# Kernel optimization log

Hardware: AMD Instinct MI355X
Metric: run time of the kernel (lower is better)

The kernel has to match this reference:

```python
import jax, jax.numpy as jnp
import numpy as np

LN_EPS = 1e-5
NEG_INF = -1e30


def setup_inputs() -> dict:
    key = jax.random.key(0)
    k_adj, k_feat, k_mask, k_w = jax.random.split(key, 4)
    B, N, H, R, L = 8, 400, 768, 46, 2
    adj = jax.random.uniform(k_adj, (B, N, N, R), dtype=jnp.float32)
    feature = jax.random.normal(k_feat, (B, N, H), dtype=jnp.float32)
    dmask = (jax.random.uniform(k_mask, (B, 1, N)) > 0.1).astype(jnp.float32)
    # per-layer, per-relation Linear(H, H, bias=False) weights, applied as x @ W
    W = jax.random.normal(k_w, (L, R, H, H), dtype=jnp.float32) / np.sqrt(H)
    return {"adj": adj, "feature": feature, "dmask": dmask, "W": W}


def reference(adj, feature, dmask, W):
    # adj: [B,N,N,R] -> [B,R,N,N]; dmask: [B,1,N] masks key/column axis
    B, N, _, R = adj.shape
    a = jnp.transpose(adj, (0, 3, 1, 2))           # [B,R,N,N]
    m = dmask[:, None, :, :]                        # [B,1,1,N]
    logits = a * m + (1.0 - m) * NEG_INF
    att = jax.nn.softmax(logits, axis=-1)           # [B,R,N,N] (layer-invariant)

    x = feature
    num_layers = W.shape[0]
    for layer in range(num_layers):
        # grouped per-relation linear: h[b,r,n,k] = feature[b,n,h] @ W[layer,r,h,k]
        h = jnp.einsum('bnh,rhk->brnk', x, W[layer])
        h = jax.nn.relu(jnp.einsum('brnm,brmk->brnk', att, h))
        addition = h.sum(axis=1)                    # sum over relations -> [B,N,H]
        z = jax.nn.relu(addition) / R
        # LayerNorm without affine params
        mu = jnp.mean(z, axis=-1, keepdims=True)
        var = jnp.var(z, axis=-1, keepdims=True)
        x = (z - mu) / jnp.sqrt(var + LN_EPS)
        # dropout is identity in eval mode
    return x
```

## Files before the change

### kernel.cpp

```cpp
#include <hip/hip_runtime.h>
#include <stdint.h>

#define BS 8
#define NN 400
#define HH 768
#define RR 46
#define MB 416
#define APAD 448
#define MFLAT2 3328
#define LDW2 3328
#define PADM 402

typedef _Float16 half8 __attribute__((ext_vector_type(8)));
typedef _Float16 half4v __attribute__((ext_vector_type(4)));
typedef float floatx4 __attribute__((ext_vector_type(4)));

__device__ __forceinline__ void async16(const void* g, void* l) {
  __builtin_amdgcn_global_load_lds((const __attribute__((address_space(1))) uint32_t*)g,
                                   (__attribute__((address_space(3))) uint32_t*)l, 16, 0, 0);
}

__device__ __forceinline__ int xcd_work(int flat, int nwg) {
  int q = nwg >> 3, rem = nwg & 7;
  int xcd = flat & 7, slot = flat >> 3;
  return (xcd < rem ? xcd * (q + 1) : rem * (q + 1) + (xcd - rem) * q) + slot;
}

__device__ __forceinline__ void vm_wait(int ahead) {
  if (ahead >= 2) asm volatile("s_waitcnt vmcnt(8)" ::: "memory");
  else if (ahead == 1) asm volatile("s_waitcnt vmcnt(4)" ::: "memory");
  else asm volatile("s_waitcnt vmcnt(0)" ::: "memory");
}
__device__ __forceinline__ void vm_wait3(int ahead) {
  if (ahead >= 2) asm volatile("s_waitcnt vmcnt(6)" ::: "memory");
  else if (ahead == 1) asm volatile("s_waitcnt vmcnt(3)" ::: "memory");
  else asm volatile("s_waitcnt vmcnt(0)" ::: "memory");
}
#define BAR_ONE() { asm volatile("s_barrier" ::: "memory"); __builtin_amdgcn_sched_barrier(0); }


__device__ __forceinline__ void mma_tiles(const _Float16* As, const _Float16* Bs, int lane,
                                          int wr, int wc, floatx4 acc[4][4]) {
  int arow = wr + (lane & 15);
  int brow = wc + (lane & 15);
  int kswz = ((lane >> 4) ^ ((lane >> 1) & 3)) * 8;
  half8 a[4], b[4];
#pragma unroll
  for (int i = 0; i < 4; ++i) a[i] = *(const half8*)&As[(arow + i * 16) * 32 + kswz];
#pragma unroll
  for (int i = 0; i < 4; ++i) b[i] = *(const half8*)&Bs[(brow + i * 16) * 32 + kswz];
#pragma unroll
  for (int i = 0; i < 4; ++i)
#pragma unroll
    for (int j = 0; j < 4; ++j)
      acc[i][j] = __builtin_amdgcn_mfma_f32_16x16x32_f16(a[i], b[j], acc[i][j], 0, 0, 0);
}

__device__ __forceinline__ void mma32(const _Float16* As, const _Float16* Bs, int lane,
                                      int wr, int wc, floatx4 acc[8][4]) {
  int arow = wr + (lane & 15);
  int brow = wc + (lane & 15);
  int kswz = ((lane >> 4) ^ ((lane >> 1) & 3)) * 8;
  half8 a[8], b[4];
#pragma unroll
  for (int i = 0; i < 8; ++i) a[i] = *(const half8*)&As[(arow + i * 16) * 32 + kswz];
#pragma unroll
  for (int j = 0; j < 4; ++j) b[j] = *(const half8*)&Bs[(brow + j * 16) * 32 + kswz];
#pragma unroll
  for (int i = 0; i < 8; ++i)
#pragma unroll
    for (int j = 0; j < 4; ++j)
      acc[i][j] = __builtin_amdgcn_mfma_f32_16x16x32_f16(a[i], b[j], acc[i][j], 0, 0, 0);
}

__global__ __launch_bounds__(256) void conv_w(const float* __restrict__ W, _Float16* __restrict__ Wt) {
  __shared__ float tl[32][33];
  int t = threadIdx.x;
  int lr = blockIdx.y;
  int tr = blockIdx.x / 24, tc = blockIdx.x % 24;
  const float* src = W + (size_t)lr * HH * HH;
  _Float16* dst = Wt + (size_t)lr * HH * HH;
  int rl = t >> 5, cl = t & 31;
#pragma unroll
  for (int j = 0; j < 4; ++j)
    tl[rl + 8 * j][cl] = src[(size_t)(tr * 32 + rl + 8 * j) * HH + tc * 32 + cl];
  __syncthreads();
#pragma unroll
  for (int j = 0; j < 4; ++j)
    dst[(size_t)(tc * 32 + rl + 8 * j) * HH + tr * 32 + cl] = (_Float16)tl[cl][rl + 8 * j];
}

__global__ void conv_x(const float* __restrict__ f, _Float16* __restrict__ x16) {
  int i4 = blockIdx.x * 256 + threadIdx.x;
  int row = i4 / 192;
  int c4 = i4 - row * 192;
  int b = row / 416;
  int m = row - b * 416;
  half4v h = {};
  if (m < NN) {
    float4 v = *(const float4*)(f + ((size_t)(b * NN + m) * HH) + c4 * 4);
    h[0] = (_Float16)v.x; h[1] = (_Float16)v.y; h[2] = (_Float16)v.z; h[3] = (_Float16)v.w;
  }
  *(half4v*)&x16[(size_t)row * HH + c4 * 4] = h;
}

__global__ __launch_bounds__(512) void att_softmax(const float* __restrict__ adj,
                                                   const float* __restrict__ dmask,
                                                   _Float16* __restrict__ att) {
  __shared__ _Float16 sE[RR * PADM];
  __shared__ float sM[NN];
  int t = threadIdx.x;
  int n = blockIdx.x, b = blockIdx.y;
  const float4* src = (const float4*)(adj + ((size_t)b * NN + n) * NN * RR);
  for (int i = t; i < NN; i += 512) sM[i] = dmask[b * NN + i];
  float4 v[9];
#pragma unroll
  for (int k = 0; k < 9; ++k) {
    int idx = t + k * 512;
    if (idx < NN * RR / 4) v[k] = src[idx];
  }
  __syncthreads();
#pragma unroll
  for (int k = 0; k < 9; ++k) {
    int idx = t + k * 512;
    if (idx < NN * RR / 4) {
      int e0 = idx * 4;
      float vv[4] = {v[k].x, v[k].y, v[k].z, v[k].w};
#pragma unroll
      for (int j = 0; j < 4; ++j) {
        int e = e0 + j;
        int m = e / RR;
        int r = e - m * RR;
        float val = sM[m] > 0.5f ? __expf(vv[j]) : 0.0f;
        sE[r * PADM + m] = (_Float16)val;
      }
    }
  }
  __syncthreads();
  int lane = t & 63, wid = t >> 6;
  for (int r = wid; r < RR; r += 8) {
    const _Float16* row = &sE[r * PADM];
    float s = 0.f;
    for (int m = lane; m < NN; m += 64) s += (float)row[m];
#pragma unroll
    for (int o = 32; o; o >>= 1) s += __shfl_xor(s, o);
    float inv = 1.0f / s;
    _Float16* orow = att + (((size_t)b * RR + r) * NN + n) * APAD;
    for (int m2 = lane * 2; m2 < APAD; m2 += 128) {
      _Float16 lo = (_Float16)0.f, hi = (_Float16)0.f;
      if (m2 < NN) lo = (_Float16)((float)row[m2] * inv);
      if (m2 + 1 < NN) hi = (_Float16)((float)row[m2 + 1] * inv);
      union { _Float16 h[2]; uint32_t u; } pk;
      pk.h[0] = lo; pk.h[1] = hi;
      *(uint32_t*)&orow[m2] = pk.u;
    }
  }
}

__global__ __launch_bounds__(512, 2) void gemm_xw(const _Float16* __restrict__ x16,
                                                  const _Float16* __restrict__ Wt,
                                                  _Float16* __restrict__ h1T, int layer, int r0, int rbase) {
  extern __shared__ __align__(16) char smraw[];
  int t = threadIdx.x;
  int work = xcd_work(blockIdx.x, gridDim.x);
  int r_i = work / 39;
  int rem = work - r_i * 39;
  int r = r0 + r_i;
  int mtile = rem / 3, ntile = rem % 3;
  const _Float16* Bp = Wt + ((size_t)layer * RR + r) * HH * HH;
  int lane = t & 63, w = t >> 6;
  int wr = (w >> 2) * 128, wc = (w & 3) * 64;
  floatx4 acc[8][4] = {};

  int c0 = w * 2;
  int swz = ((lane & 3) ^ ((lane >> 3) & 3)) * 8;
  int ra0 = mtile * 256 + c0 * 16 + (lane >> 2);
  int ra1 = ra0 + 16;
  int rb0 = ntile * 256 + c0 * 16 + (lane >> 2);
  int rb1 = rb0 + 16;
  const _Float16* pa0 = x16 + (size_t)ra0 * HH + swz;
  const _Float16* pa1 = x16 + (size_t)ra1 * HH + swz;
  const _Float16* pb0 = Bp + (size_t)rb0 * HH + swz;
  const _Float16* pb1 = Bp + (size_t)rb1 * HH + swz;
  auto issue = [&](int buf) {
    _Float16* lA = (_Float16*)(smraw + (buf << 15)) + c0 * 512;
    _Float16* lB = (_Float16*)(smraw + (buf << 15) + 16384) + c0 * 512;
    async16(pa0, lA); async16(pa1, lA + 512);
    async16(pb0, lB); async16(pb1, lB + 512);
    pa0 += 32; pa1 += 32; pb0 += 32; pb1 += 32;
  };

  issue(0); issue(1); issue(2);
  vm_wait(2);
  BAR_ONE();
  for (int s = 0; s < 24; ++s) {
    if (s + 3 < 24) issue((s + 3) & 3);
    char* cb = smraw + ((s & 3) << 15);
    __builtin_amdgcn_s_setprio(1);
    mma32((const _Float16*)cb, (const _Float16*)(cb + 16384), lane, wr, wc, acc);
    __builtin_amdgcn_s_setprio(0);
    if (s + 1 < 24) {
      int ahead = 24 - s - 2;
      vm_wait(ahead > 2 ? 2 : ahead);
      BAR_ONE();
    }
  }
  __syncthreads();

  _Float16* outl = (_Float16*)smraw + (size_t)w * 8192;
#pragma unroll
  for (int i = 0; i < 8; ++i) {
#pragma unroll
    for (int j = 0; j < 4; ++j) {
      int rl = i * 16 + (lane >> 4) * 4;
      int cl = j * 16 + (lane & 15);
      int pos = rl ^ ((cl & 7) << 3);
      half4v v = {(_Float16)acc[i][j][0], (_Float16)acc[i][j][1],
                  (_Float16)acc[i][j][2], (_Float16)acc[i][j][3]};
      *(half4v*)&outl[cl * 128 + pos] = v;
    }
  }
  _Float16* outp = h1T + (size_t)(r - rbase) * HH * LDW2;
  int gmb = mtile * 256 + wr;
  int gnb = ntile * 256 + wc;
#pragma unroll
  for (int p = 0; p < 16; ++p) {
    int c = p * 4 + (lane >> 4);
    int mq = (lane & 15) * 8;
    int mpos = mq ^ ((c & 7) << 3);
    half8 v = *(const half8*)&outl[c * 128 + mpos];
    *(half8*)&outp[(size_t)(gnb + c) * LDW2 + gmb + mq] = v;
  }
}

__global__ __launch_bounds__(512, 2) void gemm_att(const _Float16* __restrict__ att,
                                                   const _Float16* __restrict__ h1T,
                                                   float* __restrict__ partials, size_t psz,
                                                   int rs, int rcount, int rbase, int accflag,
                                                   int ngroups) {
  extern __shared__ __align__(16) char smraw[];
  int t = threadIdx.x;
  int work = xcd_work(blockIdx.x, gridDim.x);
  int ntile = work % 6;
  int tmp = work / 6;
  int mtile = tmp & 1; tmp >>= 1;
  int g = tmp % ngroups;
  int b = tmp / ngroups;
  int rbeg = rs + (g * rcount) / ngroups;
  int rend = rs + ((g + 1) * rcount) / ngroups;
  int nr = rend - rbeg;
  int total = nr * 13;
  float* part = partials + (size_t)g * psz;
  int lane = t & 63, w = t >> 6;
  int wr = (w >> 1) * 64, wc = (w & 1) * 64;
  floatx4 acc[4][4] = {}, sum[4][4] = {};

  int swz = ((lane & 3) ^ ((lane >> 3) & 3)) * 8;
  int ga0 = mtile * 256 + w * 32 + (lane >> 2);
  int ga1 = ga0 + 16;
  ga0 = ga0 > NN - 1 ? NN - 1 : ga0;
  ga1 = ga1 > NN - 1 ? NN - 1 : ga1;
  int gb = ntile * 128 + w * 16 + (lane >> 2);
  const _Float16* pa0 = att + ((size_t)b * RR + rbeg) * NN * APAD + (size_t)ga0 * APAD + swz;
  const _Float16* pa1 = att + ((size_t)b * RR + rbeg) * NN * APAD + (size_t)ga1 * APAD + swz;
  const _Float16* pb = h1T + (size_t)(rbeg - rbase) * HH * LDW2 + (size_t)gb * LDW2 + b * MB + swz;
  int nsk = 0;
  auto issue = [&](int buf) {
    _Float16* lA = (_Float16*)(smraw + buf * 24576) + (w * 2) * 512;
    _Float16* lB = (_Float16*)(smraw + buf * 24576 + 16384) + w * 512;
    async16(pa0, lA); async16(pa1, lA + 512);
    async16(pb, lB);
    if (++nsk == 13) {
      nsk = 0;
      pa0 += (size_t)NN * APAD - 384; pa1 += (size_t)NN * APAD - 384;
      pb += (size_t)HH * LDW2 - 384;
    } else { pa0 += 32; pa1 += 32; pb += 32; }
  };

  issue(0); issue(1); issue(2);
  vm_wait3(2);
  BAR_ONE();
  int cks = 0;
  for (int s = 0; s < total; ++s) {
    if (s + 3 < total) issue((s + 3) & 3);
    char* cb = smraw + (s & 3) * 24576;
    __builtin_amdgcn_s_setprio(1);
    mma_tiles((const _Float16*)cb, (const _Float16*)(cb + 16384), lane, wr, wc, acc);
    __builtin_amdgcn_s_setprio(0);
    if (cks == 12) {
#pragma unroll
      for (int i = 0; i < 4; ++i)
#pragma unroll
        for (int j = 0; j < 4; ++j) {
#pragma unroll
          for (int q2 = 0; q2 < 4; ++q2) sum[i][j][q2] += fmaxf(acc[i][j][q2], 0.0f);
          acc[i][j] = (floatx4){0.f, 0.f, 0.f, 0.f};
        }
      cks = 0;
    } else ++cks;
    if (s + 1 < total) {
      int ahead = total - s - 2;
      vm_wait3(ahead > 2 ? 2 : ahead);
      BAR_ONE();
    }
  }
#pragma unroll
  for (int i = 0; i < 4; ++i) {
    int rl = wr + i * 16 + (lane >> 4) * 4;
    int grow = mtile * 256 + rl;
#pragma unroll
    for (int j = 0; j < 4; ++j) {
      int gcol = ntile * 128 + wc + j * 16 + (lane & 15);
#pragma unroll
      for (int q2 = 0; q2 < 4; ++q2) {
        if (grow + q2 < NN) {
          size_t idx = ((size_t)b * NN + grow + q2) * HH + gcol;
          float v = sum[i][j][q2];
          if (accflag) v += part[idx];
          part[idx] = v;
        }
      }
    }
  }
}

__global__ __launch_bounds__(256) void lnorm(const float* __restrict__ partials, size_t psz, int np,
                                             _Float16* __restrict__ x16, float* __restrict__ out) {
  int row = blockIdx.x;
  int t = threadIdx.x;
  int b = row / NN;
  int xrow = row + b * 16;
  float v[3];
  float s = 0.f, s2 = 0.f;
#pragma unroll
  for (int j = 0; j < 3; ++j) {
    float a = 0.f;
    for (int gidx = 0; gidx < np; ++gidx) a += partials[(size_t)gidx * psz + (size_t)row * HH + t + j * 256];
    v[j] = fmaxf(a, 0.f) * (1.0f / RR);
    s += v[j];
    s2 += v[j] * v[j];
  }
#pragma unroll
  for (int o = 32; o; o >>= 1) {
    s += __shfl_xor(s, o);
    s2 += __shfl_xor(s2, o);
  }
  __shared__ float rs_[4], rs2_[4];
  int lane = t & 63, wid = t >> 6;
  if (!lane) { rs_[wid] = s; rs2_[wid] = s2; }
  __syncthreads();
  s = rs_[0] + rs_[1] + rs_[2] + rs_[3];
  s2 = rs2_[0] + rs2_[1] + rs2_[2] + rs2_[3];
  float mu = s * (1.0f / HH);
  float var = s2 * (1.0f / HH) - mu * mu;
  float rstd = rsqrtf(var + 1e-5f);
#pragma unroll
  for (int j = 0; j < 3; ++j) {
    float o = (v[j] - mu) * rstd;
    out[(size_t)row * HH + t + j * 256] = o;
    x16[(size_t)xrow * HH + t + j * 256] = (_Float16)o;
  }
}

extern "C" void kernel_launch(void* const* d_in, const int* in_sizes, int n_in,
                              void* d_out, int out_size, void* d_ws, size_t ws_size,
                              hipStream_t stream) {
  const float* adj = (const float*)d_in[0];
  const float* feature = (const float*)d_in[1];
  const float* dmask = (const float*)d_in[2];
  const float* W = (const float*)d_in[3];
  float* out = (float*)d_out;

  (void)hipFuncSetAttribute((const void*)gemm_xw,
                            hipFuncAttributeMaxDynamicSharedMemorySize, 131072);
  (void)hipFuncSetAttribute((const void*)gemm_att,
                            hipFuncAttributeMaxDynamicSharedMemorySize, 98304);

  uintptr_t base = (uintptr_t)d_ws;
  uintptr_t p = base;
  auto alloc = [&](size_t bytes) -> void* {
    uintptr_t q = (p + 255) & ~(uintptr_t)255;
    p = q + bytes;
    return (void*)q;
  };
  _Float16* att = (_Float16*)alloc((size_t)BS * RR * NN * APAD * 2);
  _Float16* Wt = (_Float16*)alloc((size_t)2 * RR * HH * HH * 2);
  _Float16* x16 = (_Float16*)alloc((size_t)MFLAT2 * HH * 2);
  size_t psz = (size_t)(BS * NN) * HH;
  size_t pszB = psz * 4;
  size_t used = p - base;
  size_t rem = ws_size > used ? ws_size - used : 0;
  size_t perR = (size_t)HH * LDW2 * 2;
  size_t h1full = (size_t)RR * perR;

  conv_w<<<dim3(576, 2 * RR), 256, 0, stream>>>(W, Wt);
  conv_x<<<MFLAT2 * HH / 4 / 256, 256, 0, stream>>>(feature, x16);
  att_softmax<<<dim3(NN, BS), 512, 0, stream>>>(adj, dmask, att);

  if (rem >= h1full + 4 * pszB + 512) {
    _Float16* h1T = (_Float16*)alloc(h1full);
    int ngroups = (int)(((ws_size - (p - base)) - 256) / pszB);
    if (ngroups > 8) ngroups = 8;
    float* partials = (float*)alloc((size_t)ngroups * pszB);
    for (int layer = 0; layer < 2; ++layer) {
      gemm_xw<<<39 * RR, 512, 131072, stream>>>(x16, Wt, h1T, layer, 0, 0);
      gemm_att<<<96 * ngroups, 512, 98304, stream>>>(att, h1T, partials, psz, 0, RR, 0, 0, ngroups);
      lnorm<<<BS * NN, 256, 0, stream>>>(partials, psz, ngroups, x16, out);
    }
  } else {
    float* partials = (float*)alloc(pszB);
    size_t rem2 = ws_size > (p - base) ? ws_size - (p - base) : 0;
    int RCmax = (int)(rem2 / perR);
    if (RCmax > RR) RCmax = RR;
    if (RCmax < 1) RCmax = 1;
    _Float16* h1T = (_Float16*)alloc((size_t)RCmax * perR);
    for (int layer = 0; layer < 2; ++layer) {
      for (int r0 = 0; r0 < RR; r0 += RCmax) {
        int rc = RR - r0 < RCmax ? RR - r0 : RCmax;
        gemm_xw<<<39 * rc, 512, 131072, stream>>>(x16, Wt, h1T, layer, r0, r0);
        gemm_att<<<96 * 1, 512, 98304, stream>>>(att, h1T, partials, psz, r0, rc, r0, r0 > 0, 1);
      }
      lnorm<<<BS * NN, 256, 0, stream>>>(partials, psz, 1, x16, out);
    }
  }
}
```

Baseline: 976.2 us.

## Restructure gemm_xw pipeline into half-tile stages with finer-grained async loads

Replaces the 4-buffer, per-k-step load/compute loop in gemm_xw with a pipeline that stages A and B halves separately into two 64KB slots. Each k-tile is split into half-tiles, and loads are issued interleaved between LDS fragment reads and MFMA bursts, with explicit vmcnt/lgkmcnt waits and barriers around each MFMA group. The aim is to keep more global loads in flight and overlap them better with compute. In exchange it adds more barriers per k step, and the hand-tuned waitcnt counts carry a correctness risk.

```diff
diff --git a/kernel.cpp b/kernel.cpp
--- a/kernel.cpp
+++ b/kernel.cpp
@@ -26,11 +26,6 @@
   return (xcd < rem ? xcd * (q + 1) : rem * (q + 1) + (xcd - rem) * q) + slot;
 }
 
-__device__ __forceinline__ void vm_wait(int ahead) {
-  if (ahead >= 2) asm volatile("s_waitcnt vmcnt(8)" ::: "memory");
-  else if (ahead == 1) asm volatile("s_waitcnt vmcnt(4)" ::: "memory");
-  else asm volatile("s_waitcnt vmcnt(0)" ::: "memory");
-}
 __device__ __forceinline__ void vm_wait3(int ahead) {
   if (ahead >= 2) asm volatile("s_waitcnt vmcnt(6)" ::: "memory");
   else if (ahead == 1) asm volatile("s_waitcnt vmcnt(3)" ::: "memory");
@@ -51,23 +46,6 @@
   for (int i = 0; i < 4; ++i) b[i] = *(const half8*)&Bs[(brow + i * 16) * 32 + kswz];
 #pragma unroll
   for (int i = 0; i < 4; ++i)
-#pragma unroll
-    for (int j = 0; j < 4; ++j)
-      acc[i][j] = __builtin_amdgcn_mfma_f32_16x16x32_f16(a[i], b[j], acc[i][j], 0, 0, 0);
-}
-
-__device__ __forceinline__ void mma32(const _Float16* As, const _Float16* Bs, int lane,
-                                      int wr, int wc, floatx4 acc[8][4]) {
-  int arow = wr + (lane & 15);
-  int brow = wc + (lane & 15);
-  int kswz = ((lane >> 4) ^ ((lane >> 1) & 3)) * 8;
-  half8 a[8], b[4];
-#pragma unroll
-  for (int i = 0; i < 8; ++i) a[i] = *(const half8*)&As[(arow + i * 16) * 32 + kswz];
-#pragma unroll
-  for (int j = 0; j < 4; ++j) b[j] = *(const half8*)&Bs[(brow + j * 16) * 32 + kswz];
-#pragma unroll
-  for (int i = 0; i < 8; ++i)
 #pragma unroll
     for (int j = 0; j < 4; ++j)
       acc[i][j] = __builtin_amdgcn_mfma_f32_16x16x32_f16(a[i], b[j], acc[i][j], 0, 0, 0);
@@ -172,39 +150,65 @@
   int wr = (w >> 2) * 128, wc = (w & 3) * 64;
   floatx4 acc[8][4] = {};
 
-  int c0 = w * 2;
   int swz = ((lane & 3) ^ ((lane >> 3) & 3)) * 8;
-  int ra0 = mtile * 256 + c0 * 16 + (lane >> 2);
-  int ra1 = ra0 + 16;
-  int rb0 = ntile * 256 + c0 * 16 + (lane >> 2);
-  int rb1 = rb0 + 16;
-  const _Float16* pa0 = x16 + (size_t)ra0 * HH + swz;
-  const _Float16* pa1 = x16 + (size_t)ra1 * HH + swz;
-  const _Float16* pb0 = Bp + (size_t)rb0 * HH + swz;
-  const _Float16* pb1 = Bp + (size_t)rb1 * HH + swz;
-  auto issue = [&](int buf) {
-    _Float16* lA = (_Float16*)(smraw + (buf << 15)) + c0 * 512;
-    _Float16* lB = (_Float16*)(smraw + (buf << 15) + 16384) + c0 * 512;
-    async16(pa0, lA); async16(pa1, lA + 512);
-    async16(pb0, lB); async16(pb1, lB + 512);
-    pa0 += 32; pa1 += 32; pb0 += 32; pb1 += 32;
+  int sr = t >> 2;
+  const _Float16* pa0 = x16 + (size_t)(mtile * 256 + sr) * HH + swz;
+  const _Float16* pa1 = x16 + (size_t)(mtile * 256 + sr + 128) * HH + swz;
+  const _Float16* pb0 = Bp + (size_t)(ntile * 256 + sr) * HH + swz;
+  const _Float16* pb1 = Bp + (size_t)(ntile * 256 + sr + 128) * HH + swz;
+  _Float16* dbase = (_Float16*)smraw + t * 8;
+
+  auto stage_h = [&](int h) {
+    _Float16* d = dbase + (((h >> 2) & 1) << 15) + ((h & 3) << 13);
+    if ((h & 1) == 0) { async16(pa0, d); async16(pa1, d + 4096); pa0 += 32; pa1 += 32; }
+    else             { async16(pb0, d); async16(pb1, d + 4096); pb0 += 32; pb1 += 32; }
   };
 
-  issue(0); issue(1); issue(2);
-  vm_wait(2);
+#pragma unroll
+  for (int h0 = 0; h0 < 6; ++h0) stage_h(h0);
+  asm volatile("s_waitcnt vmcnt(4)" ::: "memory");
   BAR_ONE();
-  for (int s = 0; s < 24; ++s) {
-    if (s + 3 < 24) issue((s + 3) & 3);
-    char* cb = smraw + ((s & 3) << 15);
-    __builtin_amdgcn_s_setprio(1);
-    mma32((const _Float16*)cb, (const _Float16*)(cb + 16384), lane, wr, wc, acc);
-    __builtin_amdgcn_s_setprio(0);
-    if (s + 1 < 24) {
-      int ahead = 24 - s - 2;
-      vm_wait(ahead > 2 ? 2 : ahead);
-      BAR_ONE();
-    }
-  }
+
+  int arow = wr + (lane & 15);
+  int brow = wc + (lane & 15);
+  int kswz = ((lane >> 4) ^ ((lane >> 1) & 3)) * 8;
+  int h = 6;
+  for (int kt = 0; kt < 12; ++kt) {
+    const _Float16* slot = (const _Float16*)(smraw + ((kt & 1) << 16));
+#pragma unroll
+    for (int kh = 0; kh < 2; ++kh) {
+      const _Float16* As = slot + kh * 16384;
+      const _Float16* Bs = slot + 8192 + kh * 16384;
+      half8 b[4];
+#pragma unroll
+      for (int ih = 0; ih < 2; ++ih) {
+        half8 a[4];
+#pragma unroll
+        for (int i = 0; i < 4; ++i)
+          a[i] = *(const half8*)&As[(arow + (ih * 4 + i) * 16) * 32 + kswz];
+        if (ih == 0) {
+#pragma unroll
+          for (int j = 0; j < 4; ++j)
+            b[j] = *(const half8*)&Bs[(brow + j * 16) * 32 + kswz];
+        }
+        if (h < 48) stage_h(h++);
+        asm volatile("s_waitcnt vmcnt(6)" ::: "memory");
+        BAR_ONE();
+        asm volatile("s_waitcnt lgkmcnt(0)" ::: "memory");
+        __builtin_amdgcn_sched_barrier(0);
+        __builtin_amdgcn_s_setprio(1);
+#pragma unroll
+        for (int i = 0; i < 4; ++i)
+#pragma unroll
+          for (int j = 0; j < 4; ++j)
+            acc[ih * 4 + i][j] =
+                __builtin_amdgcn_mfma_f32_16x16x32_f16(a[i], b[j], acc[ih * 4 + i][j], 0, 0, 0);
+        __builtin_amdgcn_s_setprio(0);
+        BAR_ONE();
+      }
+    }
+  }
+  asm volatile("s_waitcnt vmcnt(0)" ::: "memory");
   __syncthreads();
 
   _Float16* outl = (_Float16*)smraw + (size_t)w * 8192;
```

Measured after the change: 1.027 ms. 1.05x slower.
